# Kernel optimization log

Hardware: AMD Instinct MI355X
Metric: run time of the kernel (lower is better)

Reference implementation:

```python
import jax, jax.numpy as jnp
import numpy as np

BN_EPS = 1e-5


def setup_inputs() -> dict:
    key = jax.random.key(0)
    ks = jax.random.split(key, 10)
    N, E, D = 100000, 1600000, 64
    node_feats = jax.random.normal(ks[0], (N, D), dtype=jnp.float32)
    edge_feats = jax.random.randint(ks[1], (E, 3), 0, 2, dtype=jnp.int64)
    edge_index = jax.random.randint(ks[2], (2, E), 0, N, dtype=jnp.int64)
    return {
        "node_feats": node_feats,
        "edge_feats": edge_feats,
        "edge_index": edge_index,
        "num_nodes": N,
        "num_edges": E,
        "eps": jnp.zeros((1,), jnp.float32),
        "bond_emb0": jax.random.normal(ks[3], (5, D), dtype=jnp.float32) * 0.05,
        "bond_emb1": jax.random.normal(ks[4], (6, D), dtype=jnp.float32) * 0.05,
        "bond_emb2": jax.random.normal(ks[5], (2, D), dtype=jnp.float32) * 0.05,
        "W1": jax.random.normal(ks[6], (2 * D, D), dtype=jnp.float32) * (1.0 / np.sqrt(D)),
        "b1": jnp.zeros((2 * D,), jnp.float32),
        "gamma": jnp.ones((2 * D,), jnp.float32),
        "beta": jnp.zeros((2 * D,), jnp.float32),
        "W2": jax.random.normal(ks[7], (D, 2 * D), dtype=jnp.float32) * (1.0 / np.sqrt(2 * D)),
        "b2": jnp.zeros((D,), jnp.float32),
    }


def reference(node_feats, edge_feats, edge_index, num_nodes, num_edges,
              eps, bond_emb0, bond_emb1, bond_emb2,
              W1, b1, gamma, beta, W2, b2):
    # BondEncoder: sum of categorical embeddings over 3 bond features -> [E, D]
    edge_emb = (bond_emb0[edge_feats[:, 0]]
                + bond_emb1[edge_feats[:, 1]]
                + bond_emb2[edge_feats[:, 2]])
    # gather source-node feats (edge_index[1]), combine, relu -> [E, D]
    message = jax.nn.relu(node_feats[edge_index[1]] + edge_emb)
    # scatter_add into target nodes (edge_index[0]) -> [N, D]
    message_reduce = jax.ops.segment_sum(message, edge_index[0], num_segments=num_nodes)
    h = (1.0 + eps) * node_feats + message_reduce  # eps shape [1] broadcasts
    # MLP: Linear -> BatchNorm1d (training-mode batch stats) -> ReLU -> Linear
    h1 = h @ W1.T + b1  # [N, 2D]
    mean = jnp.mean(h1, axis=0)
    var = jnp.mean(jnp.square(h1 - mean), axis=0)  # biased variance (torch BN)
    h1 = gamma * (h1 - mean) * jax.lax.rsqrt(var + BN_EPS) + beta
    h1 = jax.nn.relu(h1)
    return h1 @ W2.T + b2  # [N, D]
```

## Files before the change

### kernel.cpp

```cpp
#include <hip/hip_runtime.h>
#include <stdint.h>

#define D   64
#define D2  128
#define R   196
#define NBK 512
#define CAP 4224

__global__ void k_embsum(
    const float* __restrict__ be0, const float* __restrict__ be1,
    const float* __restrict__ be2, float* __restrict__ embsum,
    int* __restrict__ bcursor)
{
    int c = blockIdx.x;
    int t = threadIdx.x;
    if (c < 60) {
        int f0 = c / 12;
        int r  = c % 12;
        int f1 = r / 2;
        int f2 = r % 2;
        embsum[c * D + t] = be0[f0 * D + t] + be1[f1 * D + t] + be2[f2 * D + t];
    } else {
        int i = (c - 60) * 64 + t;
        if (i < NBK) bcursor[i * 16] = i * CAP;
    }
}

__global__ __launch_bounds__(256) void k_part(
    const int* __restrict__ ei, const int* __restrict__ ef,
    int* __restrict__ bcursor, int* __restrict__ payload, int E)
{
    __shared__ int scnt[NBK];
    __shared__ int sstart[NBK];
    __shared__ int sgbase[NBK];
    __shared__ int sdat[2048];
    __shared__ unsigned short sbkt[2048];
    __shared__ int sred2[256];

    int t = threadIdx.x;
    for (int i = t; i < NBK; i += 256) scnt[i] = 0;
    __syncthreads();

    int base2 = blockIdx.x * 1024;

    int b0[4], p0[4], r0[4];
    int b1[4], p1[4], r1[4];

    #pragma unroll
    for (int k = 0; k < 4; k++) {
        int i2 = base2 + k * 256 + t;
        int e0 = i2 * 2;
        if (e0 < E) {
            int2 d  = ((const int2*)ei)[i2];
            int2 s  = ((const int2*)(ei + E))[i2];
            int2 q0 = ((const int2*)ef)[3 * i2 + 0];
            int2 q1 = ((const int2*)ef)[3 * i2 + 1];
            int2 q2 = ((const int2*)ef)[3 * i2 + 2];
            {
                int bb = d.x / R; if (bb > NBK - 1) bb = NBK - 1;
                int ld = d.x - bb * R;
                int code = q0.x * 12 + q0.y * 2 + q1.x;
                b0[k] = bb;
                p0[k] = s.x | (code << 17) | (ld << 23);
                r0[k] = atomicAdd(&scnt[bb], 1);
            }
            if (e0 + 1 < E) {
                int bb = d.y / R; if (bb > NBK - 1) bb = NBK - 1;
                int ld = d.y - bb * R;
                int code = q1.y * 12 + q2.x * 2 + q2.y;
                b1[k] = bb;
                p1[k] = s.y | (code << 17) | (ld << 23);
                r1[k] = atomicAdd(&scnt[bb], 1);
            }
        }
    }
    __syncthreads();

    int c0 = scnt[t * 2], c1 = scnt[t * 2 + 1];
    sred2[t] = c0 + c1;
    __syncthreads();
    int sv = sred2[t];
    for (int off = 1; off < 256; off <<= 1) {
        int x = (t >= off) ? sred2[t - off] : 0;
        __syncthreads();
        sred2[t] += x;
        __syncthreads();
    }
    int excl = sred2[t] - sv;
    sstart[t * 2]     = excl;
    sstart[t * 2 + 1] = excl + c0;
    __syncthreads();

    for (int i = t; i < NBK; i += 256) {
        int c = scnt[i];
        if (c) sgbase[i] = atomicAdd(&bcursor[i * 16], c);
    }
    __syncthreads();

    #pragma unroll
    for (int k = 0; k < 4; k++) {
        int i2 = base2 + k * 256 + t;
        int e0 = i2 * 2;
        if (e0 < E) {
            int slot = sstart[b0[k]] + r0[k];
            sdat[slot] = p0[k]; sbkt[slot] = (unsigned short)b0[k];
            if (e0 + 1 < E) {
                slot = sstart[b1[k]] + r1[k];
                sdat[slot] = p1[k]; sbkt[slot] = (unsigned short)b1[k];
            }
        }
    }
    __syncthreads();

    int tc = E - base2 * 2; if (tc > 2048) tc = 2048;
    #pragma unroll
    for (int k = 0; k < 8; k++) {
        int i = k * 256 + t;
        if (i < tc) {
            int bb = sbkt[i];
            int pos = sgbase[bb] + (i - sstart[bb]);
            if (pos < (bb + 1) * CAP) payload[pos] = sdat[i];
        }
    }
}

#define SME   0
#define SMP   15360
#define SMQ   32256
#define SMC   49152
#define SMU   49940
#define SMS   50724
#define SMEM_BYTES 53376

__global__ __launch_bounds__(512) void k_sortred(
    const float* __restrict__ nf,
    const int* __restrict__ bcursor,
    int* __restrict__ payload,
    const float* __restrict__ embsum,
    const float* __restrict__ epsp,
    float* __restrict__ h, int N)
{
    __shared__ __align__(16) char smem[SMEM_BYTES];
    float* sE    = (float*)(smem + SME);
    int*   sp    = (int*)(smem + SMP);
    int*   sq    = (int*)(smem + SMQ);
    int*   scn   = (int*)(smem + SMC);
    int*   scur  = (int*)(smem + SMU);
    int*   sscan = (int*)(smem + SMS);
    float* hbuf  = (float*)smem;

    int tid = threadIdx.x;
    int b = blockIdx.x;
    int n0 = b * R;

    for (int i = tid; i < 60 * D; i += 512) sE[i] = embsum[i];
    if (tid <= R) scn[tid] = 0;
    __syncthreads();

    int js = b * CAP;
    int cnt = bcursor[b * 16] - js;
    if (cnt > CAP) cnt = CAP;
    if (cnt < 0) cnt = 0;

    for (int i = tid; i < cnt; i += 512) {
        int u = payload[js + i];
        sp[i] = u;
        atomicAdd(&scn[((unsigned)u >> 23) + 1], 1);
    }
    __syncthreads();

    if (tid < 256) sscan[tid] = (tid <= R) ? scn[tid] : 0;
    __syncthreads();
    for (int off = 1; off < 256; off <<= 1) {
        int x = 0;
        if (tid < 256 && tid >= off) x = sscan[tid - off];
        __syncthreads();
        if (tid < 256) sscan[tid] += x;
        __syncthreads();
    }
    if (tid <= R) {
        scn[tid] = sscan[tid];
        if (tid < R) scur[tid] = sscan[tid];
    }
    __syncthreads();

    for (int i = tid; i < cnt; i += 512) {
        int u = sp[i];
        int pos = atomicAdd(&scur[(unsigned)u >> 23], 1);
        sq[pos] = u;
    }
    __syncthreads();

    int w = tid >> 6, l = tid & 63;
    float epsv = 1.0f + epsp[0];
    for (int r = w; r < R; r += 8) {
        int n = n0 + r;
        if (n >= N) break;
        int st = scn[r], en = scn[r + 1];
        float acc = 0.0f;
        for (int jb = st; jb < en; jb += 64) {
            int u = (jb + l < en) ? sq[jb + l] : 0;
            int m = en - jb; if (m > 64) m = 64;
            int t = 0;
            for (; t + 4 <= m; t += 4) {
                int a0 = __shfl(u, t + 0);
                int a1 = __shfl(u, t + 1);
                int a2 = __shfl(u, t + 2);
                int a3 = __shfl(u, t + 3);
                float x0 = nf[(size_t)(a0 & 0x1FFFF) * D + l];
                float x1 = nf[(size_t)(a1 & 0x1FFFF) * D + l];
                float x2 = nf[(size_t)(a2 & 0x1FFFF) * D + l];
                float x3 = nf[(size_t)(a3 & 0x1FFFF) * D + l];
                float e0 = sE[((a0 >> 17) & 63) * D + l];
                float e1 = sE[((a1 >> 17) & 63) * D + l];
                float e2 = sE[((a2 >> 17) & 63) * D + l];
                float e3 = sE[((a3 >> 17) & 63) * D + l];
                acc += fmaxf(x0 + e0, 0.0f) + fmaxf(x1 + e1, 0.0f)
                     + fmaxf(x2 + e2, 0.0f) + fmaxf(x3 + e3, 0.0f);
            }
            for (; t < m; t++) {
                int a = __shfl(u, t);
                acc += fmaxf(nf[(size_t)(a & 0x1FFFF) * D + l]
                             + sE[((a >> 17) & 63) * D + l], 0.0f);
            }
        }
        h[(size_t)n * D + l] = fmaf(epsv, nf[(size_t)n * D + l], acc);
    }
    __syncthreads();

    for (int idx = tid; idx < R * 16; idx += 512) {
        int row = idx >> 4, q = idx & 15;
        int n = n0 + row;
        float4 v = make_float4(0.0f, 0.0f, 0.0f, 0.0f);
        if (n < N) v = *(const float4*)&h[(size_t)n * D + q * 4];
        *(float4*)&hbuf[row * 68 + q * 4] = v;
    }
    __syncthreads();

    float* P = (float*)(payload + (size_t)b * CAP);
    if (tid < 256) {
        int iB = tid >> 4, jB = tid & 15;
        float M[4][4];
        #pragma unroll
        for (int a = 0; a < 4; a++)
            #pragma unroll
            for (int c = 0; c < 4; c++) M[a][c] = 0.0f;
        #pragma unroll 4
        for (int n2 = 0; n2 < R; n2++) {
            float4 a = *(const float4*)&hbuf[n2 * 68 + iB * 4];
            float4 c = *(const float4*)&hbuf[n2 * 68 + jB * 4];
            M[0][0] = fmaf(a.x, c.x, M[0][0]);
            M[0][1] = fmaf(a.x, c.y, M[0][1]);
            M[0][2] = fmaf(a.x, c.z, M[0][2]);
            M[0][3] = fmaf(a.x, c.w, M[0][3]);
            M[1][0] = fmaf(a.y, c.x, M[1][0]);
            M[1][1] = fmaf(a.y, c.y, M[1][1]);
            M[1][2] = fmaf(a.y, c.z, M[1][2]);
            M[1][3] = fmaf(a.y, c.w, M[1][3]);
            M[2][0] = fmaf(a.z, c.x, M[2][0]);
            M[2][1] = fmaf(a.z, c.y, M[2][1]);
            M[2][2] = fmaf(a.z, c.z, M[2][2]);
            M[2][3] = fmaf(a.z, c.w, M[2][3]);
            M[3][0] = fmaf(a.w, c.x, M[3][0]);
            M[3][1] = fmaf(a.w, c.y, M[3][1]);
            M[3][2] = fmaf(a.w, c.z, M[3][2]);
            M[3][3] = fmaf(a.w, c.w, M[3][3]);
        }
        #pragma unroll
        for (int a = 0; a < 4; a++)
            #pragma unroll
            for (int c = 0; c < 4; c++)
                P[(iB * 4 + a) * 64 + jB * 4 + c] = M[a][c];
    } else if (tid < 320) {
        int lc = tid - 256;
        float s = 0.0f;
        for (int r2 = 0; r2 < R; r2++) s += hbuf[r2 * 68 + lc];
        P[4096 + lc] = s;
    }
}

__global__ __launch_bounds__(256) void k_redM(
    const float* __restrict__ pM, int nblk,
    float* __restrict__ Mbar, float invN)
{
    __shared__ float sred[256];
    int tid = threadIdx.x;
    int eq = tid & 63, bq = tid >> 6;
    int e = blockIdx.x * 64 + eq;

    float s0 = 0.0f, s1 = 0.0f, s2 = 0.0f, s3 = 0.0f;
    if (e < 4160) {
        int b = bq;
        for (; b + 12 < nblk; b += 16) {
            s0 += pM[(size_t)(b +  0) * CAP + e];
            s1 += pM[(size_t)(b +  4) * CAP + e];
            s2 += pM[(size_t)(b +  8) * CAP + e];
            s3 += pM[(size_t)(b + 12) * CAP + e];
        }
        for (; b < nblk; b += 4) s0 += pM[(size_t)b * CAP + e];
    }
    sred[tid] = (s0 + s1) + (s2 + s3);
    __syncthreads();
    if (tid < 64 && e < 4160)
        Mbar[e] = (sred[tid] + sred[64 + tid] + sred[128 + tid] + sred[192 + tid]) * invN;
}

__global__ void k_bn(
    const float* __restrict__ Mbar,
    const float* __restrict__ W1,
    const float* __restrict__ b1,
    const float* __restrict__ gamma, const float* __restrict__ beta,
    float* __restrict__ ss)
{
    __shared__ float sMb[4160];
    int tid = threadIdx.x;
    for (int i = tid; i < 4160; i += 128) sMb[i] = Mbar[i];
    __syncthreads();

    int c = tid;
    float w[64];
    #pragma unroll
    for (int k = 0; k < 64; k++) w[k] = W1[c * D + k];

    float d = 0.0f;
    #pragma unroll
    for (int k = 0; k < 64; k++) d = fmaf(w[k], sMb[4096 + k], d);

    float Q = 0.0f;
    for (int k = 0; k < 64; k++) {
        float tk = 0.0f;
        #pragma unroll
        for (int j = 0; j < 64; j++) tk = fmaf(sMb[k * 64 + j], w[j], tk);
        Q = fmaf(w[k], tk, Q);
    }

    float var  = fmaxf(Q - d * d, 0.0f);
    float mean = d + b1[c];
    float sc   = gamma[c] * rsqrtf(var + 1e-5f);
    ss[c]       = sc;
    ss[128 + c] = beta[c] - mean * sc;
}

__global__ __launch_bounds__(256) void k_gemm2(
    const float* __restrict__ h,
    const float* __restrict__ W1,
    const float* __restrict__ b1,
    const float* __restrict__ ss,
    const float* __restrict__ W2,
    const float* __restrict__ b2v,
    float* __restrict__ out,
    int N, int tiles)
{
    __shared__ float AB[32 * 128];
    __shared__ float W1t[64 * 128];
    __shared__ float W2t[128 * 64];

    int tid = threadIdx.x;
    int ty = tid >> 5, tx = tid & 31;

    {
        int c  = tid >> 1;
        int k0 = (tid & 1) * 32;
        const float4* wr = (const float4*)(W1 + c * D + k0);
        #pragma unroll
        for (int q = 0; q < 8; q++) {
            float4 u = wr[q];
            int k = k0 + q * 4;
            W1t[(k + 0) * 128 + c] = u.x;
            W1t[(k + 1) * 128 + c] = u.y;
            W1t[(k + 2) * 128 + c] = u.z;
            W1t[(k + 3) * 128 + c] = u.w;
        }
    }
    {
        int j  = tid >> 2;
        int k0 = (tid & 3) * 32;
        const float4* wr = (const float4*)(W2 + j * D2 + k0);
        #pragma unroll
        for (int q = 0; q < 8; q++) {
            float4 u = wr[q];
            int k = k0 + q * 4;
            W2t[(k + 0) * 64 + j] = u.x;
            W2t[(k + 1) * 64 + j] = u.y;
            W2t[(k + 2) * 64 + j] = u.z;
            W2t[(k + 3) * 64 + j] = u.w;
        }
    }

    float bb0 = b1[tx * 4 + 0];
    float bb1 = b1[tx * 4 + 1];
    float bb2 = b1[tx * 4 + 2];
    float bb3 = b1[tx * 4 + 3];
    float4 scv = *(const float4*)&ss[tx * 4];
    float4 shv = *(const float4*)&ss[128 + tx * 4];
    float ob0 = b2v[tx * 2 + 0];
    float ob1 = b2v[tx * 2 + 1];

    for (int t = blockIdx.x; t < tiles; t += gridDim.x) {
        int row0 = t * 32;
        __syncthreads();
        {
            int r  = tid >> 3;
            int c8 = (tid & 7) * 8;
            int gr = row0 + r;
            float* dstp = &AB[r * 128 + c8];
            if (gr < N) {
                const float4* hrow = (const float4*)(h + (size_t)gr * D + c8);
                ((float4*)dstp)[0] = hrow[0];
                ((float4*)dstp)[1] = hrow[1];
            } else {
                #pragma unroll
                for (int m = 0; m < 8; m++) dstp[m] = 0.0f;
            }
        }
        __syncthreads();

        float acc[4][4];
        #pragma unroll
        for (int i = 0; i < 4; i++)
            #pragma unroll
            for (int j = 0; j < 4; j++) acc[i][j] = 0.0f;

        #pragma unroll 4
        for (int k4 = 0; k4 < 16; k4++) {
            float4 w0 = *(const float4*)&W1t[(k4 * 4 + 0) * 128 + tx * 4];
            float4 w1 = *(const float4*)&W1t[(k4 * 4 + 1) * 128 + tx * 4];
            float4 w2 = *(const float4*)&W1t[(k4 * 4 + 2) * 128 + tx * 4];
            float4 w3 = *(const float4*)&W1t[(k4 * 4 + 3) * 128 + tx * 4];
            #pragma unroll
            for (int i = 0; i < 4; i++) {
                float4 a = *(const float4*)&AB[(ty * 4 + i) * 128 + k4 * 4];
                acc[i][0] = fmaf(a.x, w0.x, acc[i][0]);
                acc[i][1] = fmaf(a.x, w0.y, acc[i][1]);
                acc[i][2] = fmaf(a.x, w0.z, acc[i][2]);
                acc[i][3] = fmaf(a.x, w0.w, acc[i][3]);
                acc[i][0] = fmaf(a.y, w1.x, acc[i][0]);
                acc[i][1] = fmaf(a.y, w1.y, acc[i][1]);
                acc[i][2] = fmaf(a.y, w1.z, acc[i][2]);
                acc[i][3] = fmaf(a.y, w1.w, acc[i][3]);
                acc[i][0] = fmaf(a.z, w2.x, acc[i][0]);
                acc[i][1] = fmaf(a.z, w2.y, acc[i][1]);
                acc[i][2] = fmaf(a.z, w2.z, acc[i][2]);
                acc[i][3] = fmaf(a.z, w2.w, acc[i][3]);
                acc[i][0] = fmaf(a.w, w3.x, acc[i][0]);
                acc[i][1] = fmaf(a.w, w3.y, acc[i][1]);
                acc[i][2] = fmaf(a.w, w3.z, acc[i][2]);
                acc[i][3] = fmaf(a.w, w3.w, acc[i][3]);
            }
        }
        __syncthreads();

        #pragma unroll
        for (int i = 0; i < 4; i++) {
            float g0 = fmaxf(fmaf(acc[i][0] + bb0, scv.x, shv.x), 0.0f);
            float g1 = fmaxf(fmaf(acc[i][1] + bb1, scv.y, shv.y), 0.0f);
            float g2 = fmaxf(fmaf(acc[i][2] + bb2, scv.z, shv.z), 0.0f);
            float g3 = fmaxf(fmaf(acc[i][3] + bb3, scv.w, shv.w), 0.0f);
            *(float4*)&AB[(ty * 4 + i) * 128 + tx * 4] = make_float4(g0, g1, g2, g3);
        }
        __syncthreads();

        float acc2[4][2];
        #pragma unroll
        for (int i = 0; i < 4; i++) { acc2[i][0] = 0.0f; acc2[i][1] = 0.0f; }

        #pragma unroll 4
        for (int k4 = 0; k4 < 32; k4++) {
            float2 u0 = *(const float2*)&W2t[(k4 * 4 + 0) * 64 + tx * 2];
            float2 u1 = *(const float2*)&W2t[(k4 * 4 + 1) * 64 + tx * 2];
            float2 u2 = *(const float2*)&W2t[(k4 * 4 + 2) * 64 + tx * 2];
            float2 u3 = *(const float2*)&W2t[(k4 * 4 + 3) * 64 + tx * 2];
            #pragma unroll
            for (int i = 0; i < 4; i++) {
                float4 b = *(const float4*)&AB[(ty * 4 + i) * 128 + k4 * 4];
                acc2[i][0] = fmaf(b.x, u0.x, acc2[i][0]);
                acc2[i][1] = fmaf(b.x, u0.y, acc2[i][1]);
                acc2[i][0] = fmaf(b.y, u1.x, acc2[i][0]);
                acc2[i][1] = fmaf(b.y, u1.y, acc2[i][1]);
                acc2[i][0] = fmaf(b.z, u2.x, acc2[i][0]);
                acc2[i][1] = fmaf(b.z, u2.y, acc2[i][1]);
                acc2[i][0] = fmaf(b.w, u3.x, acc2[i][0]);
                acc2[i][1] = fmaf(b.w, u3.y, acc2[i][1]);
            }
        }

        #pragma unroll
        for (int i = 0; i < 4; i++) {
            int gr = row0 + ty * 4 + i;
            if (gr < N) {
                float2 pk = make_float2(acc2[i][0] + ob0, acc2[i][1] + ob1);
                ((float2*)out)[(size_t)gr * 32 + tx] = pk;
            }
        }
    }
}

extern "C" void kernel_launch(void* const* d_in, const int* in_sizes, int n_in,
                              void* d_out, int out_size, void* d_ws, size_t ws_size,
                              hipStream_t stream)
{
    const float* nf    = (const float*)d_in[0];
    const int*   ef    = (const int*)d_in[1];
    const int*   ei    = (const int*)d_in[2];
    const float* epsp  = (const float*)d_in[5];
    const float* be0   = (const float*)d_in[6];
    const float* be1   = (const float*)d_in[7];
    const float* be2   = (const float*)d_in[8];
    const float* W1    = (const float*)d_in[9];
    const float* b1    = (const float*)d_in[10];
    const float* gamma = (const float*)d_in[11];
    const float* beta  = (const float*)d_in[12];
    const float* W2    = (const float*)d_in[13];
    const float* b2v   = (const float*)d_in[14];
    float*       out   = (float*)d_out;

    int N = in_sizes[0] / D;
    int E = in_sizes[1] / 3;

    int tiles2 = (N + 31) / 32;
    int g2 = 512;

    float* h       = (float*)d_ws;
    float* Mbar    = h + (size_t)N * D;
    float* ss      = Mbar + 4160;
    float* embsum  = ss + 256;
    int*   bcursor = (int*)(embsum + 60 * D);
    int*   payload = bcursor + NBK * 16;
    float* pM      = (float*)payload;

    k_embsum<<<68, 64, 0, stream>>>(be0, be1, be2, embsum, bcursor);

    int E2 = (E + 1) / 2;
    int gP = (E2 + 1023) / 1024;
    k_part<<<gP, 256, 0, stream>>>(ei, ef, bcursor, payload, E);

    k_sortred<<<NBK, 512, 0, stream>>>(nf, bcursor, payload, embsum, epsp, h, N);

    k_redM<<<65, 256, 0, stream>>>(pM, NBK, Mbar, 1.0f / (float)N);
    k_bn<<<1, 128, 0, stream>>>(Mbar, W1, b1, gamma, beta, ss);

    k_gemm2<<<g2, 256, 0, stream>>>(h, W1, b1, ss, W2, b2v, out, N, tiles2);
}
```

Before: 370.1 us.

## Halve bucket size, store symmetric Gram triangle, retile GEMM to 64-row tiles

The node buckets are halved (R=98, NBK=1024) to give more, smaller blocks with lower shared-memory use and an occupancy hint for the sort-reduce kernel. The staging of payload into shared memory and of h into an LDS buffer is dropped, so those values are re-read from global memory. The per-block Gram matrix now stores only its upper triangle, which halves the partial-sum traffic reduced by k_redM. The fused MLP kernel moves to 64-row tiles with padded LDS rows and reads W2 directly from global memory instead of a transposed LDS copy. These choices trade LDS capacity and bank conflicts against extra global reads and register pressure.

```diff
diff --git a/kernel.cpp b/kernel.cpp
--- a/kernel.cpp
+++ b/kernel.cpp
@@ -1,11 +1,12 @@
 #include <hip/hip_runtime.h>
 #include <stdint.h>
 
-#define D   64
-#define D2  128
-#define R   196
-#define NBK 512
-#define CAP 4224
+#define D    64
+#define D2   128
+#define R    98
+#define NBK  1024
+#define CAP  2176
+#define NTRI 2144
 
 __global__ void k_embsum(
     const float* __restrict__ be0, const float* __restrict__ be1,
@@ -76,8 +77,10 @@
     }
     __syncthreads();
 
-    int c0 = scnt[t * 2], c1 = scnt[t * 2 + 1];
-    sred2[t] = c0 + c1;
+    int loc[4]; int s = 0;
+    #pragma unroll
+    for (int k = 0; k < 4; k++) { loc[k] = s; s += scnt[t * 4 + k]; }
+    sred2[t] = s;
     __syncthreads();
     int sv = sred2[t];
     for (int off = 1; off < 256; off <<= 1) {
@@ -87,8 +90,8 @@
         __syncthreads();
     }
     int excl = sred2[t] - sv;
-    sstart[t * 2]     = excl;
-    sstart[t * 2 + 1] = excl + c0;
+    #pragma unroll
+    for (int k = 0; k < 4; k++) sstart[t * 4 + k] = excl + loc[k];
     __syncthreads();
 
     for (int i = t; i < NBK; i += 256) {
@@ -124,15 +127,7 @@
     }
 }
 
-#define SME   0
-#define SMP   15360
-#define SMQ   32256
-#define SMC   49152
-#define SMU   49940
-#define SMS   50724
-#define SMEM_BYTES 53376
-
-__global__ __launch_bounds__(512) void k_sortred(
+__global__ __launch_bounds__(512, 8) void k_sortred(
     const float* __restrict__ nf,
     const int* __restrict__ bcursor,
     int* __restrict__ payload,
@@ -140,14 +135,11 @@
     const float* __restrict__ epsp,
     float* __restrict__ h, int N)
 {
-    __shared__ __align__(16) char smem[SMEM_BYTES];
-    float* sE    = (float*)(smem + SME);
-    int*   sp    = (int*)(smem + SMP);
-    int*   sq    = (int*)(smem + SMQ);
-    int*   scn   = (int*)(smem + SMC);
-    int*   scur  = (int*)(smem + SMU);
-    int*   sscan = (int*)(smem + SMS);
-    float* hbuf  = (float*)smem;
+    __shared__ float sE[60 * D];
+    __shared__ int   sq[CAP];
+    __shared__ int   scn[R + 1];
+    __shared__ int   scur[R];
+    __shared__ int   sscan[128];
 
     int tid = threadIdx.x;
     int b = blockIdx.x;
@@ -162,20 +154,17 @@
     if (cnt > CAP) cnt = CAP;
     if (cnt < 0) cnt = 0;
 
-    for (int i = tid; i < cnt; i += 512) {
-        int u = payload[js + i];
-        sp[i] = u;
-        atomicAdd(&scn[((unsigned)u >> 23) + 1], 1);
-    }
-    __syncthreads();
-
-    if (tid < 256) sscan[tid] = (tid <= R) ? scn[tid] : 0;
-    __syncthreads();
-    for (int off = 1; off < 256; off <<= 1) {
+    for (int i = tid; i < cnt; i += 512)
+        atomicAdd(&scn[((unsigned)payload[js + i] >> 23) + 1], 1);
+    __syncthreads();
+
+    if (tid < 128) sscan[tid] = (tid <= R) ? scn[tid] : 0;
+    __syncthreads();
+    for (int off = 1; off < 128; off <<= 1) {
         int x = 0;
-        if (tid < 256 && tid >= off) x = sscan[tid - off];
-        __syncthreads();
-        if (tid < 256) sscan[tid] += x;
+        if (tid < 128 && tid >= off) x = sscan[tid - off];
+        __syncthreads();
+        if (tid < 128) sscan[tid] += x;
         __syncthreads();
     }
     if (tid <= R) {
@@ -185,7 +174,7 @@
     __syncthreads();
 
     for (int i = tid; i < cnt; i += 512) {
-        int u = sp[i];
+        int u = payload[js + i];
         int pos = atomicAdd(&scur[(unsigned)u >> 23], 1);
         sq[pos] = u;
     }
@@ -228,16 +217,8 @@
     }
     __syncthreads();
 
-    for (int idx = tid; idx < R * 16; idx += 512) {
-        int row = idx >> 4, q = idx & 15;
-        int n = n0 + row;
-        float4 v = make_float4(0.0f, 0.0f, 0.0f, 0.0f);
-        if (n < N) v = *(const float4*)&h[(size_t)n * D + q * 4];
-        *(float4*)&hbuf[row * 68 + q * 4] = v;
-    }
-    __syncthreads();
-
     float* P = (float*)(payload + (size_t)b * CAP);
+    const float4* h4 = (const float4*)h;
     if (tid < 256) {
         int iB = tid >> 4, jB = tid & 15;
         float M[4][4];
@@ -245,10 +226,12 @@
         for (int a = 0; a < 4; a++)
             #pragma unroll
             for (int c = 0; c < 4; c++) M[a][c] = 0.0f;
-        #pragma unroll 4
+        #pragma unroll 2
         for (int n2 = 0; n2 < R; n2++) {
-            float4 a = *(const float4*)&hbuf[n2 * 68 + iB * 4];
-            float4 c = *(const float4*)&hbuf[n2 * 68 + jB * 4];
+            int n = n0 + n2;
+            if (n >= N) break;
+            float4 a = h4[(size_t)n * 16 + iB];
+            float4 c = h4[(size_t)n * 16 + jB];
             M[0][0] = fmaf(a.x, c.x, M[0][0]);
             M[0][1] = fmaf(a.x, c.y, M[0][1]);
             M[0][2] = fmaf(a.x, c.z, M[0][2]);
@@ -269,40 +252,51 @@
         #pragma unroll
         for (int a = 0; a < 4; a++)
             #pragma unroll
-            for (int c = 0; c < 4; c++)
-                P[(iB * 4 + a) * 64 + jB * 4 + c] = M[a][c];
+            for (int c = 0; c < 4; c++) {
+                int gi = iB * 4 + a, gj = jB * 4 + c;
+                if (gi <= gj)
+                    P[gi * 64 + gj - ((gi * (gi + 1)) >> 1)] = M[a][c];
+            }
     } else if (tid < 320) {
         int lc = tid - 256;
         float s = 0.0f;
-        for (int r2 = 0; r2 < R; r2++) s += hbuf[r2 * 68 + lc];
-        P[4096 + lc] = s;
-    }
-}
-
-__global__ __launch_bounds__(256) void k_redM(
+        for (int n2 = 0; n2 < R; n2++) {
+            int n = n0 + n2;
+            if (n >= N) break;
+            s += h[(size_t)n * D + lc];
+        }
+        P[2080 + lc] = s;
+    }
+}
+
+__global__ __launch_bounds__(512) void k_redM(
     const float* __restrict__ pM, int nblk,
     float* __restrict__ Mbar, float invN)
 {
-    __shared__ float sred[256];
+    __shared__ float sred[512];
     int tid = threadIdx.x;
     int eq = tid & 63, bq = tid >> 6;
     int e = blockIdx.x * 64 + eq;
 
     float s0 = 0.0f, s1 = 0.0f, s2 = 0.0f, s3 = 0.0f;
-    if (e < 4160) {
+    if (e < NTRI) {
         int b = bq;
-        for (; b + 12 < nblk; b += 16) {
+        for (; b + 24 < nblk; b += 32) {
             s0 += pM[(size_t)(b +  0) * CAP + e];
-            s1 += pM[(size_t)(b +  4) * CAP + e];
-            s2 += pM[(size_t)(b +  8) * CAP + e];
-            s3 += pM[(size_t)(b + 12) * CAP + e];
-        }
-        for (; b < nblk; b += 4) s0 += pM[(size_t)b * CAP + e];
+            s1 += pM[(size_t)(b +  8) * CAP + e];
+            s2 += pM[(size_t)(b + 16) * CAP + e];
+            s3 += pM[(size_t)(b + 24) * CAP + e];
+        }
+        for (; b < nblk; b += 8) s0 += pM[(size_t)b * CAP + e];
     }
     sred[tid] = (s0 + s1) + (s2 + s3);
     __syncthreads();
-    if (tid < 64 && e < 4160)
-        Mbar[e] = (sred[tid] + sred[64 + tid] + sred[128 + tid] + sred[192 + tid]) * invN;
+    if (tid < 64 && e < NTRI) {
+        float s = 0.0f;
+        #pragma unroll
+        for (int q = 0; q < 8; q++) s += sred[q * 64 + tid];
+        Mbar[e] = s * invN;
+    }
 }
 
 __global__ void k_bn(
@@ -314,7 +308,13 @@
 {
     __shared__ float sMb[4160];
     int tid = threadIdx.x;
-    for (int i = tid; i < 4160; i += 128) sMb[i] = Mbar[i];
+    for (int idx = tid; idx < 4096; idx += 128) {
+        int i = idx >> 6, j = idx & 63;
+        int a = i < j ? i : j;
+        int b = i < j ? j : i;
+        sMb[idx] = Mbar[a * 64 + b - ((a * (a + 1)) >> 1)];
+    }
+    if (tid < 64) sMb[4096 + tid] = Mbar[2080 + tid];
     __syncthreads();
 
     int c = tid;
@@ -341,6 +341,7 @@
     ss[128 + c] = beta[c] - mean * sc;
 }
 
+#define ABS 132
 __global__ __launch_bounds__(256) void k_gemm2(
     const float* __restrict__ h,
     const float* __restrict__ W1,
@@ -351,9 +352,8 @@
     float* __restrict__ out,
     int N, int tiles)
 {
-    __shared__ float AB[32 * 128];
+    __shared__ float AB[64 * ABS];
     __shared__ float W1t[64 * 128];
-    __shared__ float W2t[128 * 64];
 
     int tid = threadIdx.x;
     int ty = tid >> 5, tx = tid & 31;
@@ -372,20 +372,6 @@
             W1t[(k + 3) * 128 + c] = u.w;
         }
     }
-    {
-        int j  = tid >> 2;
-        int k0 = (tid & 3) * 32;
-        const float4* wr = (const float4*)(W2 + j * D2 + k0);
-        #pragma unroll
-        for (int q = 0; q < 8; q++) {
-            float4 u = wr[q];
-            int k = k0 + q * 4;
-            W2t[(k + 0) * 64 + j] = u.x;
-            W2t[(k + 1) * 64 + j] = u.y;
-            W2t[(k + 2) * 64 + j] = u.z;
-            W2t[(k + 3) * 64 + j] = u.w;
-        }
-    }
 
     float bb0 = b1[tx * 4 + 0];
     float bb1 = b1[tx * 4 + 1];
@@ -393,31 +379,33 @@
     float bb3 = b1[tx * 4 + 3];
     float4 scv = *(const float4*)&ss[tx * 4];
     float4 shv = *(const float4*)&ss[128 + tx * 4];
-    float ob0 = b2v[tx * 2 + 0];
-    float ob1 = b2v[tx * 2 + 1];
+
+    int r2g = tid >> 4;
+    int c2g = tid & 15;
+    float4 obv = *(const float4*)&b2v[c2g * 4];
 
     for (int t = blockIdx.x; t < tiles; t += gridDim.x) {
-        int row0 = t * 32;
+        int row0 = t * 64;
         __syncthreads();
         {
-            int r  = tid >> 3;
-            int c8 = (tid & 7) * 8;
-            int gr = row0 + r;
-            float* dstp = &AB[r * 128 + c8];
+            int r   = tid >> 2;
+            int c16 = (tid & 3) * 16;
+            int gr  = row0 + r;
+            float* dstp = &AB[r * ABS + c16];
             if (gr < N) {
-                const float4* hrow = (const float4*)(h + (size_t)gr * D + c8);
-                ((float4*)dstp)[0] = hrow[0];
-                ((float4*)dstp)[1] = hrow[1];
+                const float4* hrow = (const float4*)(h + (size_t)gr * D + c16);
+                #pragma unroll
+                for (int m = 0; m < 4; m++) ((float4*)dstp)[m] = hrow[m];
             } else {
                 #pragma unroll
-                for (int m = 0; m < 8; m++) dstp[m] = 0.0f;
-            }
-        }
-        __syncthreads();
-
-        float acc[4][4];
-        #pragma unroll
-        for (int i = 0; i < 4; i++)
+                for (int m = 0; m < 16; m++) dstp[m] = 0.0f;
+            }
+        }
+        __syncthreads();
+
+        float acc[8][4];
+        #pragma unroll
+        for (int i = 0; i < 8; i++)
             #pragma unroll
             for (int j = 0; j < 4; j++) acc[i][j] = 0.0f;
 
@@ -428,8 +416,8 @@
             float4 w2 = *(const float4*)&W1t[(k4 * 4 + 2) * 128 + tx * 4];
             float4 w3 = *(const float4*)&W1t[(k4 * 4 + 3) * 128 + tx * 4];
             #pragma unroll
-            for (int i = 0; i < 4; i++) {
-                float4 a = *(const float4*)&AB[(ty * 4 + i) * 128 + k4 * 4];
+            for (int i = 0; i < 8; i++) {
+                float4 a = *(const float4*)&AB[(ty * 8 + i) * ABS + k4 * 4];
                 acc[i][0] = fmaf(a.x, w0.x, acc[i][0]);
                 acc[i][1] = fmaf(a.x, w0.y, acc[i][1]);
                 acc[i][2] = fmaf(a.x, w0.z, acc[i][2]);
@@ -451,45 +439,56 @@
         __syncthreads();
 
         #pragma unroll
-        for (int i = 0; i < 4; i++) {
+        for (int i = 0; i < 8; i++) {
             float g0 = fmaxf(fmaf(acc[i][0] + bb0, scv.x, shv.x), 0.0f);
             float g1 = fmaxf(fmaf(acc[i][1] + bb1, scv.y, shv.y), 0.0f);
             float g2 = fmaxf(fmaf(acc[i][2] + bb2, scv.z, shv.z), 0.0f);
             float g3 = fmaxf(fmaf(acc[i][3] + bb3, scv.w, shv.w), 0.0f);
-            *(float4*)&AB[(ty * 4 + i) * 128 + tx * 4] = make_float4(g0, g1, g2, g3);
-        }
-        __syncthreads();
-
-        float acc2[4][2];
-        #pragma unroll
-        for (int i = 0; i < 4; i++) { acc2[i][0] = 0.0f; acc2[i][1] = 0.0f; }
+            *(float4*)&AB[(ty * 8 + i) * ABS + tx * 4] = make_float4(g0, g1, g2, g3);
+        }
+        __syncthreads();
+
+        float acc2[4][4];
+        #pragma unroll
+        for (int i = 0; i < 4; i++)
+            #pragma unroll
+            for (int j = 0; j < 4; j++) acc2[i][j] = 0.0f;
 
         #pragma unroll 4
         for (int k4 = 0; k4 < 32; k4++) {
-            float2 u0 = *(const float2*)&W2t[(k4 * 4 + 0) * 64 + tx * 2];
-            float2 u1 = *(const float2*)&W2t[(k4 * 4 + 1) * 64 + tx * 2];
-            float2 u2 = *(const float2*)&W2t[(k4 * 4 + 2) * 64 + tx * 2];
-            float2 u3 = *(const float2*)&W2t[(k4 * 4 + 3) * 64 + tx * 2];
+            float4 u0 = *(const float4*)&W2[(c2g * 4 + 0) * D2 + k4 * 4];
+            float4 u1 = *(const float4*)&W2[(c2g * 4 + 1) * D2 + k4 * 4];
+            float4 u2 = *(const float4*)&W2[(c2g * 4 + 2) * D2 + k4 * 4];
+            float4 u3 = *(const float4*)&W2[(c2g * 4 + 3) * D2 + k4 * 4];
             #pragma unroll
             for (int i = 0; i < 4; i++) {
-                float4 b = *(const float4*)&AB[(ty * 4 + i) * 128 + k4 * 4];
-                acc2[i][0] = fmaf(b.x, u0.x, acc2[i][0]);
-                acc2[i][1] = fmaf(b.x, u0.y, acc2[i][1]);
-                acc2[i][0] = fmaf(b.y, u1.x, acc2[i][0]);
-                acc2[i][1] = fmaf(b.y, u1.y, acc2[i][1]);
-                acc2[i][0] = fmaf(b.z, u2.x, acc2[i][0]);
-                acc2[i][1] = fmaf(b.z, u2.y, acc2[i][1]);
-                acc2[i][0] = fmaf(b.w, u3.x, acc2[i][0]);
-                acc2[i][1] = fmaf(b.w, u3.y, acc2[i][1]);
+                float4 g = *(const float4*)&AB[(r2g * 4 + i) * ABS + k4 * 4];
+                acc2[i][0] = fmaf(g.x, u0.x, acc2[i][0]);
+                acc2[i][1] = fmaf(g.x, u1.x, acc2[i][1]);
+                acc2[i][2] = fmaf(g.x, u2.x, acc2[i][2]);
+                acc2[i][3] = fmaf(g.x, u3.x, acc2[i][3]);
+                acc2[i][0] = fmaf(g.y, u0.y, acc2[i][0]);
+                acc2[i][1] = fmaf(g.y, u1.y, acc2[i][1]);
+                acc2[i][2] = fmaf(g.y, u2.y, acc2[i][2]);
+                acc2[i][3] = fmaf(g.y, u3.y, acc2[i][3]);
+                acc2[i][0] = fmaf(g.z, u0.z, acc2[i][0]);
+                acc2[i][1] = fmaf(g.z, u1.z, acc2[i][1]);
+                acc2[i][2] = fmaf(g.z, u2.z, acc2[i][2]);
+                acc2[i][3] = fmaf(g.z, u3.z, acc2[i][3]);
+                acc2[i][0] = fmaf(g.w, u0.w, acc2[i][0]);
+                acc2[i][1] = fmaf(g.w, u1.w, acc2[i][1]);
+                acc2[i][2] = fmaf(g.w, u2.w, acc2[i][2]);
+                acc2[i][3] = fmaf(g.w, u3.w, acc2[i][3]);
             }
         }
 
         #pragma unroll
         for (int i = 0; i < 4; i++) {
-            int gr = row0 + ty * 4 + i;
+            int gr = row0 + r2g * 4 + i;
             if (gr < N) {
-                float2 pk = make_float2(acc2[i][0] + ob0, acc2[i][1] + ob1);
-                ((float2*)out)[(size_t)gr * 32 + tx] = pk;
+                float4 pk = make_float4(acc2[i][0] + obv.x, acc2[i][1] + obv.y,
+                                        acc2[i][2] + obv.z, acc2[i][3] + obv.w);
+                *(float4*)&out[(size_t)gr * D + c2g * 4] = pk;
             }
         }
     }
@@ -517,18 +516,18 @@
     int N = in_sizes[0] / D;
     int E = in_sizes[1] / 3;
 
-    int tiles2 = (N + 31) / 32;
+    int tiles2 = (N + 63) / 64;
     int g2 = 512;
 
     float* h       = (float*)d_ws;
     float* Mbar    = h + (size_t)N * D;
-    float* ss      = Mbar + 4160;
+    float* ss      = Mbar + 2176;
     float* embsum  = ss + 256;
     int*   bcursor = (int*)(embsum + 60 * D);
     int*   payload = bcursor + NBK * 16;
     float* pM      = (float*)payload;
 
-    k_embsum<<<68, 64, 0, stream>>>(be0, be1, be2, embsum, bcursor);
+    k_embsum<<<76, 64, 0, stream>>>(be0, be1, be2, embsum, bcursor);
 
     int E2 = (E + 1) / 2;
     int gP = (E2 + 1023) / 1024;
@@ -536,7 +535,7 @@
 
     k_sortred<<<NBK, 512, 0, stream>>>(nf, bcursor, payload, embsum, epsp, h, N);
 
-    k_redM<<<65, 256, 0, stream>>>(pM, NBK, Mbar, 1.0f / (float)N);
+    k_redM<<<(NTRI + 63) / 64, 512, 0, stream>>>(pM, NBK, Mbar, 1.0f / (float)N);
     k_bn<<<1, 128, 0, stream>>>(Mbar, W1, b1, gamma, beta, ss);
 
     k_gemm2<<<g2, 256, 0, stream>>>(h, W1, b1, ss, W2, b2v, out, N, tiles2);
```

Result: slower. 452.2 us (+22.2%).
